# Kernel tuning notes

Measured on AMD Instinct MI355X. Metric: run time of the kernel, lower is better.

## Reference

```python
import jax, jax.numpy as jnp
import numpy as np
from jax import lax

N, C, RC, H, W = 2, 256, 32, 64, 64  # RC = C // 8


def conv1x1(x, w, b):
    # x: [n,c,h,w], w: [o,c], b: [o]
    return jnp.einsum('nchw,oc->nohw', x, w) + b[None, :, None, None]


def conv3x3(x, w, b):
    # x: [n,c,h,w], w: [o,i,3,3]
    y = lax.conv_general_dilated(x, w, window_strides=(1, 1), padding='SAME',
                                 dimension_numbers=('NCHW', 'OIHW', 'NCHW'))
    return y + b[None, :, None, None]


def setup_inputs() -> dict:
    key = jax.random.key(0)
    ks = jax.random.split(key, 16)
    p = lambda k, s: jax.random.normal(k, s, dtype=jnp.float32) * 0.02
    z = lambda o: jnp.zeros((o,), jnp.float32)
    return {
        'rgb_feat': jax.random.normal(ks[0], (N, C, H, W), jnp.float32),
        'chm_feat': jax.random.normal(ks[1], (N, C, H, W), jnp.float32),
        'rgb_q_w': p(ks[2], (RC, C)), 'rgb_q_b': z(RC),
        'rgb_k_w': p(ks[3], (RC, C)), 'rgb_k_b': z(RC),
        'rgb_v_w': p(ks[4], (C, C)), 'rgb_v_b': z(C),
        'depth_q_w': p(ks[5], (RC, C)), 'depth_q_b': z(RC),
        'depth_k_w': p(ks[6], (RC, C)), 'depth_k_b': z(RC),
        'depth_v_w': p(ks[7], (C, C)), 'depth_v_b': z(C),
        'gate_w': p(ks[8], (C, 2 * C)), 'gate_b': z(C),
        'fus1_w': p(ks[9], (2 * C, 2 * C)), 'fus1_b': z(2 * C),
        'fus2_w': p(ks[10], (2 * C, 2 * C, 3, 3)), 'fus2_b': z(2 * C),
        'fus3_w': p(ks[11], (C, 2 * C)), 'fus3_b': z(C),
        'skip_w': p(ks[12], (C, 2 * C)), 'skip_b': z(C),
    }


def reference(rgb_feat, chm_feat,
              rgb_q_w, rgb_q_b, rgb_k_w, rgb_k_b, rgb_v_w, rgb_v_b,
              depth_q_w, depth_q_b, depth_k_w, depth_k_b, depth_v_w, depth_v_b,
              gate_w, gate_b, fus1_w, fus1_b, fus2_w, fus2_b,
              fus3_w, fus3_b, skip_w, skip_b):
    n, c, h, w = rgb_feat.shape
    hw = h * w
    flat = lambda t: t.reshape(n, t.shape[1], hw)

    rq = flat(conv1x1(rgb_feat, rgb_q_w, rgb_q_b))       # [n,rc,hw]
    rk = flat(conv1x1(rgb_feat, rgb_k_w, rgb_k_b))       # [n,rc,hw]
    rv = flat(conv1x1(rgb_feat, rgb_v_w, rgb_v_b))       # [n,c,hw]
    dq = flat(conv1x1(chm_feat, depth_q_w, depth_q_b))   # [n,rc,hw]
    dk = flat(conv1x1(chm_feat, depth_k_w, depth_k_b))   # [n,rc,hw]
    dv = flat(conv1x1(chm_feat, depth_v_w, depth_v_b))   # [n,c,hw]

    # rgb branch attended with depth-derived attention
    rgb_attn = jax.nn.softmax(jnp.einsum('nri,nrj->nij', dq, dk), axis=-1)  # [n,hw,hw]
    br = jnp.einsum('nci,nij->ncj', rv, rgb_attn).reshape(rgb_feat.shape) + rgb_feat

    # depth branch attended with rgb-derived attention
    depth_attn = jax.nn.softmax(jnp.einsum('nri,nrj->nij', rq, rk), axis=-1)
    bd = jnp.einsum('nci,nij->ncj', dv, depth_attn).reshape(chm_feat.shape) + chm_feat

    cat = jnp.concatenate([br, bd], axis=1)              # [n,2c,h,w]
    g = jax.nn.sigmoid(conv1x1(cat, gate_w, gate_b))     # [n,c,h,w]
    c_fused = br * g + bd * (1.0 - g)
    d_fused = br * bd
    f = jnp.concatenate([c_fused, d_fused], axis=1)      # [n,2c,h,w]

    y = jax.nn.relu(conv1x1(f, fus1_w, fus1_b))
    y = jax.nn.relu(conv3x3(y, fus2_w, fus2_b))
    y = conv1x1(y, fus3_w, fus3_b)
    fused = y + conv1x1(f, skip_w, skip_b)
    return fused
```

## Files before the change

### kernel.cpp

```cpp
#include <hip/hip_runtime.h>
#include <stdint.h>


typedef __bf16 bf16_t;
typedef __bf16 bf16x8 __attribute__((ext_vector_type(8)));
typedef float f32x4 __attribute__((ext_vector_type(4)));

#define HW 4096
#define NB 2

__device__ inline f32x4 mfma_bf16(bf16x8 a, bf16x8 b, f32x4 c) {
    return __builtin_amdgcn_mfma_f32_16x16x32_bf16(a, b, c, 0, 0, 0);
}

#define MAXJOB 12
struct CvtJobs {
    const float* src[MAXJOB];
    bf16_t* dst[MAXJOB];
    int vend[MAXJOB];
    int rowlen[MAXJOB];
    int rowstride[MAXJOB];
    int rowoff[MAXJOB];
};

__global__ __launch_bounds__(256) void convert_batch_k(CvtJobs J, int totalvec) {
    int gv = blockIdx.x * 256 + threadIdx.x;
    if (gv >= totalvec) return;
    int j = 0;
    while (gv >= J.vend[j]) j++;
    int vbase = (j == 0) ? 0 : J.vend[j - 1];
    int e = (gv - vbase) * 8;
    const float* s = J.src[j] + e;
    float4 f0 = *(const float4*)s;
    float4 f1 = *(const float4*)(s + 4);
    bf16x8 o;
    o[0] = (bf16_t)f0.x; o[1] = (bf16_t)f0.y; o[2] = (bf16_t)f0.z; o[3] = (bf16_t)f0.w;
    o[4] = (bf16_t)f1.x; o[5] = (bf16_t)f1.y; o[6] = (bf16_t)f1.z; o[7] = (bf16_t)f1.w;
    int di = e;
    if (J.rowlen[j])
        di = (e / J.rowlen[j]) * J.rowstride[j] + J.rowoff[j] + (e % J.rowlen[j]);
    *(bf16x8*)(J.dst[j] + di) = o;
}

__global__ __launch_bounds__(256) void pack_bias_k(const float* qr, const float* kr,
                                                   const float* qd, const float* kd,
                                                   const float* sb, const float* fb,
                                                   float* BQK_R, float* BQK_D, float* BSUM) {
    int t = threadIdx.x;
    if (t < 32) {
        BQK_R[t] = qr[t]; BQK_R[32 + t] = kr[t];
        BQK_D[t] = qd[t]; BQK_D[32 + t] = kd[t];
    }
    BSUM[t] = sb[t] + fb[t];
}

__global__ __launch_bounds__(256) void reorder_fus2_k(const float* __restrict__ src,
                                                      bf16_t* __restrict__ dst) {
    int idx = blockIdx.x * 256 + threadIdx.x;
    if (idx >= 512 * 4608) return;
    int o = idx / 4608;
    int t = idx % 4608;
    int t9 = t / 512;
    int c  = t % 512;
    dst[idx] = (bf16_t)src[(size_t)o * 4608 + c * 9 + t9];
}

template <int EPI, bool OUT_BF16>
__global__ __launch_bounds__(256) void gemm_k(const bf16_t* __restrict__ A,
                                              const bf16_t* __restrict__ A2,
                                              const bf16_t* __restrict__ B,
                                              const float* __restrict__ bias,
                                              const float* __restrict__ bias2,
                                              void* __restrict__ outp,
                                              const void* __restrict__ aux,
                                              int M, int K, size_t strideB, size_t strideO) {
    __shared__ bf16_t Bt[64][72];
    const int t = threadIdx.x;
    const int mb = blockIdx.x, jb = blockIdx.y, n = blockIdx.z;
    const int w = t >> 6, lane = t & 63, quad = lane >> 4, l16 = lane & 15;

    const bf16_t* Au = (n >= 2) ? A2 : A;
    const float* biasu = (n >= 2) ? bias2 : bias;

    const bf16_t* Bb = B + (size_t)n * strideB + jb * 64;
    const int srow = t >> 2;
    const int scol = (t & 3) << 4;

    f32x4 zero = {0.f, 0.f, 0.f, 0.f};
    f32x4 acc[4] = {zero, zero, zero, zero};

    const bf16_t* Arow = Au + (size_t)(mb * 64 + w * 16 + l16) * K + quad * 8;

    for (int k0 = 0; k0 < K; k0 += 64) {
        const bf16_t* src = Bb + (size_t)(k0 + srow) * HW + scol;
        bf16x8 v0 = *(const bf16x8*)src;
        bf16x8 v1 = *(const bf16x8*)(src + 8);
        __syncthreads();
#pragma unroll
        for (int e = 0; e < 8; e++) Bt[scol + e][srow] = v0[e];
#pragma unroll
        for (int e = 0; e < 8; e++) Bt[scol + 8 + e][srow] = v1[e];
        __syncthreads();

        bf16x8 a0 = *(const bf16x8*)(Arow + k0);
        bf16x8 a1 = *(const bf16x8*)(Arow + k0 + 32);
#pragma unroll
        for (int ns = 0; ns < 4; ns++) {
            bf16x8 b0 = *(const bf16x8*)&Bt[ns * 16 + l16][quad * 8];
            bf16x8 b1 = *(const bf16x8*)&Bt[ns * 16 + l16][32 + quad * 8];
            acc[ns] = mfma_bf16(a0, b0, acc[ns]);
            acc[ns] = mfma_bf16(a1, b1, acc[ns]);
        }
    }

    if (EPI == 6) {
#pragma unroll
        for (int ns = 0; ns < 4; ns++) {
            int col = jb * 64 + ns * 16 + l16;
            union { bf16_t h[4]; unsigned long long u; } pk;
#pragma unroll
            for (int rr = 0; rr < 4; rr++) {
                int m = w * 16 + quad * 4 + rr;
                pk.h[rr] = (bf16_t)(acc[ns][rr] + biasu[m]);
            }
            *(unsigned long long*)((bf16_t*)outp +
                ((size_t)n * HW + col) * 64 + w * 16 + quad * 4) = pk.u;
        }
    } else if (EPI == 7) {
        const int m_base = mb * 64 + w * 16 + quad * 4;
#pragma unroll
        for (int ns = 0; ns < 4; ns++) {
            int col = jb * 64 + ns * 16 + l16;
            union { bf16_t h[4]; unsigned long long u; } pk;
#pragma unroll
            for (int rr = 0; rr < 4; rr++) {
                float v = acc[ns][rr] + biasu[m_base + rr];
                pk.h[rr] = (bf16_t)(v > 0.f ? v : 0.f);
            }
            *(unsigned long long*)((bf16_t*)outp +
                ((size_t)n * HW + col) * 512 + m_base) = pk.u;
        }
    } else if (EPI == 5) {
        const bf16_t* catp = (const bf16_t*)aux;
        bf16_t* f = (bf16_t*)outp;
#pragma unroll
        for (int ns = 0; ns < 4; ns++) {
#pragma unroll
            for (int rr = 0; rr < 4; rr++) {
                int m = mb * 64 + w * 16 + quad * 4 + rr;
                int col = jb * 64 + ns * 16 + l16;
                float v = acc[ns][rr] + biasu[m];
                float g = 1.f / (1.f + __expf(-v));
                size_t base = (size_t)n * 512 * HW + (size_t)m * HW + col;
                float br = (float)catp[base];
                float bd = (float)catp[base + (size_t)256 * HW];
                size_t ob = (size_t)n * 1024 * HW + (size_t)m * HW + col;
                f[ob] = (bf16_t)(br * g + bd * (1.f - g));
                f[ob + (size_t)256 * HW] = (bf16_t)(br * bd);
            }
        }
    } else {
#pragma unroll
        for (int ns = 0; ns < 4; ns++) {
#pragma unroll
            for (int rr = 0; rr < 4; rr++) {
                int m = mb * 64 + w * 16 + quad * 4 + rr;
                int col = jb * 64 + ns * 16 + l16;
                float v = acc[ns][rr] + biasu[m];
                if (EPI == 1) v = v > 0.f ? v : 0.f;
                size_t oi = (size_t)n * strideO + (size_t)m * HW + col;
                if (OUT_BF16) ((bf16_t*)outp)[oi] = (bf16_t)v;
                else ((float*)outp)[oi] = v;
            }
        }
    }
}

__global__ __launch_bounds__(256) void conv3_k(const bf16_t* __restrict__ A,
                                               const bf16_t* __restrict__ Y1n,
                                               const float* __restrict__ bias,
                                               bf16_t* __restrict__ outp,
                                               size_t strideN) {
    __shared__ bf16_t kTn[198][72];
    const int t = threadIdx.x;
    const int mb = blockIdx.x, y = blockIdx.y, n = blockIdx.z;
    const int w = t >> 6, lane = t & 63, quad = lane >> 4, l16 = lane & 15;

    f32x4 zero = {0.f, 0.f, 0.f, 0.f};
    f32x4 acc[2][4];
#pragma unroll
    for (int i = 0; i < 2; i++)
#pragma unroll
        for (int j = 0; j < 4; j++) acc[i][j] = zero;

    const bf16_t* Yb = Y1n + (size_t)n * HW * 512;

    const bf16_t* Arow0 = A + (size_t)(mb * 128 + w * 32 + l16) * 4608 + quad * 8;
    const bf16_t* Arow1 = Arow0 + (size_t)16 * 4608;

    int pxs[7], seg[7], gidx[7];
    bool ok[7], act[7];
#pragma unroll
    for (int i = 0; i < 7; i++) {
        int slot = t + i * 256;
        act[i] = slot < 1584;
        int ps = act[i] ? (slot >> 3) : 0;
        pxs[i] = ps;
        seg[i] = slot & 7;
        int r = ps / 66, xm = ps % 66;
        int yy = y + r - 1, xx = xm - 1;
        ok[i] = act[i] && ((unsigned)yy < 64u) && ((unsigned)xx < 64u);
        gidx[i] = ok[i] ? (yy * 64 + xx) : 0;
    }

    for (int c0 = 0; c0 < 512; c0 += 64) {
        bf16x8 vals[7];
#pragma unroll
        for (int i = 0; i < 7; i++) {
            bf16x8 v;
            if (ok[i]) {
                v = *(const bf16x8*)(Yb + (size_t)gidx[i] * 512 + c0 + seg[i] * 8);
            } else {
#pragma unroll
                for (int e = 0; e < 8; e++) v[e] = (bf16_t)0.f;
            }
            vals[i] = v;
        }
        __syncthreads();
#pragma unroll
        for (int i = 0; i < 7; i++)
            if (act[i]) *(bf16x8*)&kTn[pxs[i]][seg[i] * 8] = vals[i];
        __syncthreads();

#pragma unroll
        for (int t9 = 0; t9 < 9; t9++) {
            const int dy = t9 / 3, dx = t9 % 3;
            const bf16_t* ap0 = Arow0 + t9 * 512 + c0;
            const bf16_t* ap1 = Arow1 + t9 * 512 + c0;
            bf16x8 a00 = *(const bf16x8*)(ap0);
            bf16x8 a01 = *(const bf16x8*)(ap0 + 32);
            bf16x8 a10 = *(const bf16x8*)(ap1);
            bf16x8 a11 = *(const bf16x8*)(ap1 + 32);
#pragma unroll
            for (int ns = 0; ns < 4; ns++) {
                int p = dy * 66 + ns * 16 + l16 + dx;
                bf16x8 b0 = *(const bf16x8*)&kTn[p][quad * 8];
                bf16x8 b1 = *(const bf16x8*)&kTn[p][32 + quad * 8];
                acc[0][ns] = mfma_bf16(a00, b0, acc[0][ns]);
                acc[0][ns] = mfma_bf16(a01, b1, acc[0][ns]);
                acc[1][ns] = mfma_bf16(a10, b0, acc[1][ns]);
                acc[1][ns] = mfma_bf16(a11, b1, acc[1][ns]);
            }
        }
    }

#pragma unroll
    for (int ms = 0; ms < 2; ms++) {
#pragma unroll
        for (int ns = 0; ns < 4; ns++) {
#pragma unroll
            for (int rr = 0; rr < 4; rr++) {
                int m = mb * 128 + w * 32 + ms * 16 + quad * 4 + rr;
                int x = ns * 16 + l16;
                float v = acc[ms][ns][rr] + bias[m];
                v = v > 0.f ? v : 0.f;
                outp[(size_t)n * strideN + (size_t)m * HW + y * 64 + x] = (bf16_t)v;
            }
        }
    }
}

#define ATTN_STEP(P, AS, AV, ASN, AVN, ITN)                                    \
    {                                                                          \
        _Pragma("unroll")                                                      \
        for (int ns = 0; ns < 2; ns++) {                                       \
            f32x4 s = mfma_bf16(AS, bS[ns], zero);                             \
            union { bf16_t h[4]; unsigned long long u; } pk;                   \
            float zs = 0.f;                                                    \
            _Pragma("unroll")                                                  \
            for (int rr = 0; rr < 4; rr++) {                                   \
                pk.h[rr] = (bf16_t)__expf(s[rr]);                              \
                zs += (float)pk.h[rr];                                         \
            }                                                                  \
            zacc[ns] += zs;                                                    \
            *(unsigned long long*)&PT[P][ns * 16 + l16][w * 16 + quad * 4] = pk.u; \
        }                                                                      \
        ASN = *(const bf16x8*)(Qa + (size_t)(ITN) * (128 * 64));               \
        _Pragma("unroll")                                                      \
        for (int ks = 0; ks < 4; ks++) {                                       \
            AVN[0][ks] = *(const bf16x8*)(Vr0 + (size_t)(ITN) * 128 + ks * 32);\
            AVN[1][ks] = *(const bf16x8*)(Vr1 + (size_t)(ITN) * 128 + ks * 32);\
        }                                                                      \
        asm volatile("s_waitcnt lgkmcnt(0)" ::: "memory");                     \
        __builtin_amdgcn_s_barrier();                                          \
        __builtin_amdgcn_sched_barrier(0);                                     \
        __builtin_amdgcn_s_setprio(1);                                         \
        _Pragma("unroll")                                                      \
        for (int ns = 0; ns < 2; ns++) {                                       \
            _Pragma("unroll")                                                  \
            for (int ks = 0; ks < 4; ks++) {                                   \
                bf16x8 b = *(const bf16x8*)&PT[P][ns * 16 + l16][ks * 32 + quad * 8]; \
                acc[0][ns] = mfma_bf16(AV[0][ks], b, acc[0][ns]);              \
                acc[1][ns] = mfma_bf16(AV[1][ks], b, acc[1][ns]);              \
            }                                                                  \
        }                                                                      \
        __builtin_amdgcn_s_setprio(0);                                         \
    }

__global__ __launch_bounds__(512) void attn3_k(const bf16_t* __restrict__ QKT,
                                               const bf16_t* __restrict__ V,
                                               const float* __restrict__ rgb_feat,
                                               const float* __restrict__ chm_feat,
                                               bf16_t* __restrict__ CAT) {
    __shared__ bf16_t PT[2][32][136];
    __shared__ float Zp[8][32];
    const int t = threadIdx.x;
    const int lin = blockIdx.x + (blockIdx.y << 7);
    const int z = (lin >> 1) & 3;
    const int jb = ((lin >> 3) << 1) | (lin & 1);
    const int w = t >> 6, lane = t & 63, quad = lane >> 4, l16 = lane & 15;
    const int qs = z ^ 2, n = z & 1;

    const bf16_t* Q = QKT + (size_t)qs * HW * 64;

    bf16x8 bS[2];
#pragma unroll
    for (int ns = 0; ns < 2; ns++)
        bS[ns] = *(const bf16x8*)(Q + (size_t)(jb * 32 + ns * 16 + l16) * 64 + 32 + quad * 8);

    f32x4 zero = {0.f, 0.f, 0.f, 0.f};
    f32x4 acc[2][2];
#pragma unroll
    for (int i = 0; i < 2; i++)
#pragma unroll
        for (int j = 0; j < 2; j++) acc[i][j] = zero;
    float zacc[2] = {0.f, 0.f};

    const bf16_t* Vr0 = V + ((size_t)z * 256 + w * 16 + l16) * HW + quad * 8;
    const bf16_t* Vr1 = Vr0 + (size_t)128 * HW;
    const bf16_t* Qa = Q + (size_t)(w * 16 + l16) * 64 + quad * 8;

    bf16x8 aS0, aS1, aV0[2][4], aV1[2][4];
    aS0 = *(const bf16x8*)Qa;
#pragma unroll
    for (int ks = 0; ks < 4; ks++) {
        aV0[0][ks] = *(const bf16x8*)(Vr0 + ks * 32);
        aV0[1][ks] = *(const bf16x8*)(Vr1 + ks * 32);
    }

    for (int ii = 0; ii < 16; ii++) {
        const int it0 = 2 * ii;
        ATTN_STEP(0, aS0, aV0, aS1, aV1, it0 + 1);
        ATTN_STEP(1, aS1, aV1, aS0, aV0, (it0 + 2) & 31);
    }

#pragma unroll
    for (int ns = 0; ns < 2; ns++) {
        zacc[ns] += __shfl_xor(zacc[ns], 16, 64);
        zacc[ns] += __shfl_xor(zacc[ns], 32, 64);
    }
    if (lane < 16) { Zp[w][lane] = zacc[0]; Zp[w][16 + lane] = zacc[1]; }
    __syncthreads();
    float rz[2];
#pragma unroll
    for (int ns = 0; ns < 2; ns++) {
        float ssum = 0.f;
#pragma unroll
        for (int ww = 0; ww < 8; ww++) ssum += Zp[ww][ns * 16 + l16];
        rz[ns] = 1.f / ssum;
    }

    const float* feat = ((z < 2) ? rgb_feat : chm_feat) + (size_t)n * 256 * HW;
    bf16_t* outp = CAT + (size_t)n * 512 * HW + (size_t)(z < 2 ? 0 : 256) * HW;
#pragma unroll
    for (int ct = 0; ct < 2; ct++) {
#pragma unroll
        for (int ns = 0; ns < 2; ns++) {
#pragma unroll
            for (int rr = 0; rr < 4; rr++) {
                int c = ct * 128 + w * 16 + quad * 4 + rr;
                int col = jb * 32 + ns * 16 + l16;
                float v = acc[ct][ns][rr] * rz[ns] + feat[(size_t)c * HW + col];
                outp[(size_t)c * HW + col] = (bf16_t)v;
            }
        }
    }
}

extern "C" void kernel_launch(void* const* d_in, const int* in_sizes, int n_in,
                              void* d_out, int out_size, void* d_ws, size_t ws_size,
                              hipStream_t stream) {
    (void)in_sizes; (void)n_in; (void)out_size; (void)ws_size;

    const float* rgb_feat  = (const float*)d_in[0];
    const float* chm_feat  = (const float*)d_in[1];
    const float* rgb_q_w   = (const float*)d_in[2];
    const float* rgb_q_b   = (const float*)d_in[3];
    const float* rgb_k_w   = (const float*)d_in[4];
    const float* rgb_k_b   = (const float*)d_in[5];
    const float* rgb_v_w   = (const float*)d_in[6];
    const float* rgb_v_b   = (const float*)d_in[7];
    const float* depth_q_w = (const float*)d_in[8];
    const float* depth_q_b = (const float*)d_in[9];
    const float* depth_k_w = (const float*)d_in[10];
    const float* depth_k_b = (const float*)d_in[11];
    const float* depth_v_w = (const float*)d_in[12];
    const float* depth_v_b = (const float*)d_in[13];
    const float* gate_w    = (const float*)d_in[14];
    const float* gate_b    = (const float*)d_in[15];
    const float* fus1_w    = (const float*)d_in[16];
    const float* fus1_b    = (const float*)d_in[17];
    const float* fus2_w    = (const float*)d_in[18];
    const float* fus2_b    = (const float*)d_in[19];
    const float* fus3_w    = (const float*)d_in[20];
    const float* fus3_b    = (const float*)d_in[21];
    const float* skip_w    = (const float*)d_in[22];
    const float* skip_b    = (const float*)d_in[23];

    char* ws = (char*)d_ws;
    size_t off = 0;
    auto alloc = [&](size_t bytes) -> char* {
        char* p = ws + off;
        off += (bytes + 255) & ~(size_t)255;
        return p;
    };

    bf16_t* WQK_R = (bf16_t*)alloc(64 * 256 * 2);
    bf16_t* WQK_D = (bf16_t*)alloc(64 * 256 * 2);
    bf16_t* WV_R  = (bf16_t*)alloc(256 * 256 * 2);
    bf16_t* WV_D  = (bf16_t*)alloc(256 * 256 * 2);
    bf16_t* WGATE = (bf16_t*)alloc(256 * 512 * 2);
    bf16_t* WFUS1 = (bf16_t*)alloc(512 * 512 * 2);
    bf16_t* WFUS2 = (bf16_t*)alloc(512 * 4608 * 2);
    bf16_t* WCAT  = (bf16_t*)alloc(256 * 1024 * 2);
    float*  BQK_R = (float*)alloc(64 * 4);
    float*  BQK_D = (float*)alloc(64 * 4);
    float*  BSUM  = (float*)alloc(256 * 4);
    bf16_t* XB    = (bf16_t*)alloc((size_t)4 * 256 * HW * 2);
    bf16_t* QKT   = (bf16_t*)alloc((size_t)4 * HW * 64 * 2);
    bf16_t* V4    = (bf16_t*)alloc((size_t)4 * 256 * HW * 2);
    bf16_t* CAT   = (bf16_t*)alloc((size_t)NB * 512 * HW * 2);
    bf16_t* FY    = (bf16_t*)alloc((size_t)NB * 1024 * HW * 2);
    bf16_t* Y1    = (bf16_t*)alloc((size_t)NB * HW * 512 * 2);

    bf16_t* XR = XB;
    bf16_t* XC = XB + (size_t)2 * 256 * HW;

    CvtJobs J;
    int cum = 0, nj = 0;
    auto addjob = [&](const float* s, bf16_t* d, int cnt, int rl, int rs, int ro) {
        J.src[nj] = s; J.dst[nj] = d; cum += cnt / 8; J.vend[nj] = cum;
        J.rowlen[nj] = rl; J.rowstride[nj] = rs; J.rowoff[nj] = ro; nj++;
    };
    addjob(rgb_feat, XR, NB * 256 * HW, 0, 0, 0);
    addjob(chm_feat, XC, NB * 256 * HW, 0, 0, 0);
    addjob(rgb_q_w, WQK_R, 32 * 256, 0, 0, 0);
    addjob(rgb_k_w, WQK_R + 32 * 256, 32 * 256, 0, 0, 0);
    addjob(depth_q_w, WQK_D, 32 * 256, 0, 0, 0);
    addjob(depth_k_w, WQK_D + 32 * 256, 32 * 256, 0, 0, 0);
    addjob(rgb_v_w, WV_R, 256 * 256, 0, 0, 0);
    addjob(depth_v_w, WV_D, 256 * 256, 0, 0, 0);
    addjob(gate_w, WGATE, 256 * 512, 0, 0, 0);
    addjob(fus1_w, WFUS1, 512 * 512, 0, 0, 0);
    addjob(skip_w, WCAT, 256 * 512, 512, 1024, 0);
    addjob(fus3_w, WCAT, 256 * 512, 512, 1024, 512);
    int totalvec = cum;
    convert_batch_k<<<dim3((totalvec + 255) / 256), 256, 0, stream>>>(J, totalvec);
    reorder_fus2_k<<<dim3(512 * 4608 / 256), 256, 0, stream>>>(fus2_w, WFUS2);
    pack_bias_k<<<dim3(1), 256, 0, stream>>>(rgb_q_b, rgb_k_b, depth_q_b, depth_k_b,
                                             skip_b, fus3_b, BQK_R, BQK_D, BSUM);

    gemm_k<6, true><<<dim3(1, 64, 4), 256, 0, stream>>>(
        WQK_R, WQK_D, XB, BQK_R, BQK_D, QKT, nullptr, 64, 256, (size_t)256 * HW, 0);

    gemm_k<0, true><<<dim3(4, 64, 4), 256, 0, stream>>>(
        WV_R, WV_D, XB, rgb_v_b, depth_v_b, V4, nullptr, 256, 256, (size_t)256 * HW, (size_t)256 * HW);

    attn3_k<<<dim3(128, 4), 512, 0, stream>>>(QKT, V4, rgb_feat, chm_feat, CAT);

    gemm_k<5, true><<<dim3(4, 64, NB), 256, 0, stream>>>(
        WGATE, WGATE, CAT, gate_b, gate_b, FY, CAT, 256, 512, (size_t)512 * HW, 0);

    gemm_k<7, true><<<dim3(8, 64, NB), 256, 0, stream>>>(
        WFUS1, WFUS1, FY, fus1_b, fus1_b, Y1, nullptr, 512, 512, (size_t)1024 * HW, 0);

    conv3_k<<<dim3(4, 64, NB), 256, 0, stream>>>(WFUS2, Y1, fus2_b,
                                                 FY + (size_t)512 * HW, (size_t)1024 * HW);

    gemm_k<0, false><<<dim3(4, 64, NB), 256, 0, stream>>>(
        WCAT, WCAT, FY, BSUM, BSUM, d_out, nullptr, 256, 1024, (size_t)1024 * HW, (size_t)256 * HW);
}
```

Measured before the change: 401.5 us.

## Restructure attention kernel to split keys across waves, keeping P in registers

The attention kernel now gives each wave a contiguous quarter of the key range. It feeds the exponentiated scores straight from registers into 16x16x16 MFMAs, so the shared-memory round trip and the per-step barrier on P go away. Channels are split into two halves across twice as many 256-thread blocks. The per-wave partial outputs are reduced through a float shared-memory buffer at the end. In exchange, scores are recomputed once per channel half, register pressure rises (16 accumulators plus V prefetch), and a cross-wave reduction epilogue is added.

```diff
diff --git a/kernel.cpp b/kernel.cpp
--- a/kernel.cpp
+++ b/kernel.cpp
@@ -5,12 +5,16 @@
 typedef __bf16 bf16_t;
 typedef __bf16 bf16x8 __attribute__((ext_vector_type(8)));
 typedef float f32x4 __attribute__((ext_vector_type(4)));
+typedef short s16x4 __attribute__((ext_vector_type(4)));
 
 #define HW 4096
 #define NB 2
 
 __device__ inline f32x4 mfma_bf16(bf16x8 a, bf16x8 b, f32x4 c) {
     return __builtin_amdgcn_mfma_f32_16x16x32_bf16(a, b, c, 0, 0, 0);
+}
+__device__ inline f32x4 mfma16(s16x4 a, s16x4 b, f32x4 c) {
+    return __builtin_amdgcn_mfma_f32_16x16x16bf16_1k(a, b, c, 0, 0, 0);
 }
 
 #define MAXJOB 12
@@ -270,54 +274,51 @@
     }
 }
 
-#define ATTN_STEP(P, AS, AV, ASN, AVN, ITN)                                    \
-    {                                                                          \
-        _Pragma("unroll")                                                      \
-        for (int ns = 0; ns < 2; ns++) {                                       \
-            f32x4 s = mfma_bf16(AS, bS[ns], zero);                             \
-            union { bf16_t h[4]; unsigned long long u; } pk;                   \
-            float zs = 0.f;                                                    \
-            _Pragma("unroll")                                                  \
-            for (int rr = 0; rr < 4; rr++) {                                   \
-                pk.h[rr] = (bf16_t)__expf(s[rr]);                              \
-                zs += (float)pk.h[rr];                                         \
-            }                                                                  \
-            zacc[ns] += zs;                                                    \
-            *(unsigned long long*)&PT[P][ns * 16 + l16][w * 16 + quad * 4] = pk.u; \
-        }                                                                      \
-        ASN = *(const bf16x8*)(Qa + (size_t)(ITN) * (128 * 64));               \
-        _Pragma("unroll")                                                      \
-        for (int ks = 0; ks < 4; ks++) {                                       \
-            AVN[0][ks] = *(const bf16x8*)(Vr0 + (size_t)(ITN) * 128 + ks * 32);\
-            AVN[1][ks] = *(const bf16x8*)(Vr1 + (size_t)(ITN) * 128 + ks * 32);\
-        }                                                                      \
-        asm volatile("s_waitcnt lgkmcnt(0)" ::: "memory");                     \
-        __builtin_amdgcn_s_barrier();                                          \
-        __builtin_amdgcn_sched_barrier(0);                                     \
-        __builtin_amdgcn_s_setprio(1);                                         \
-        _Pragma("unroll")                                                      \
-        for (int ns = 0; ns < 2; ns++) {                                       \
-            _Pragma("unroll")                                                  \
-            for (int ks = 0; ks < 4; ks++) {                                   \
-                bf16x8 b = *(const bf16x8*)&PT[P][ns * 16 + l16][ks * 32 + quad * 8]; \
-                acc[0][ns] = mfma_bf16(AV[0][ks], b, acc[0][ns]);              \
-                acc[1][ns] = mfma_bf16(AV[1][ks], b, acc[1][ns]);              \
-            }                                                                  \
-        }                                                                      \
-        __builtin_amdgcn_s_setprio(0);                                         \
-    }
-
-__global__ __launch_bounds__(512) void attn3_k(const bf16_t* __restrict__ QKT,
+#define SSTEP(AS, SV)                                                          \
+    { SV[0] = mfma_bf16(AS, bS[0], zero); SV[1] = mfma_bf16(AS, bS[1], zero); }
+
+#define EXPPACK(SV, PB)                                                        \
+    { _Pragma("unroll")                                                        \
+      for (int ns = 0; ns < 2; ns++) {                                         \
+          union { bf16_t h[4]; s16x4 v; } pk;                                  \
+          float zs = 0.f;                                                      \
+          _Pragma("unroll")                                                    \
+          for (int rr = 0; rr < 4; rr++) {                                     \
+              pk.h[rr] = (bf16_t)__expf(SV[ns][rr]);                           \
+              zs += (float)pk.h[rr];                                           \
+          }                                                                    \
+          zacc[ns] += zs;                                                      \
+          PB[ns] = pk.v;                                                       \
+      } }
+
+#define PV16(AV, PB)                                                           \
+    { __builtin_amdgcn_s_setprio(1);                                           \
+      _Pragma("unroll")                                                        \
+      for (int ci = 0; ci < 8; ci++) {                                         \
+          acc[ci][0] = mfma16(AV[ci], PB[0], acc[ci][0]);                      \
+          acc[ci][1] = mfma16(AV[ci], PB[1], acc[ci][1]);                      \
+      }                                                                        \
+      __builtin_amdgcn_s_setprio(0); }
+
+#define LOADQ(DST, T) DST = *(const bf16x8*)(Qa + (size_t)((T) & 63) * (16 * 64));
+
+#define LOADV(DST, T)                                                          \
+    { _Pragma("unroll")                                                        \
+      for (int ci = 0; ci < 8; ci++)                                           \
+          DST[ci] = *(const s16x4*)(Vq + (size_t)ci * (16 * HW) + ((T) & 63) * 16); }
+
+__global__ __launch_bounds__(256) void attn3_k(const bf16_t* __restrict__ QKT,
                                                const bf16_t* __restrict__ V,
                                                const float* __restrict__ rgb_feat,
                                                const float* __restrict__ chm_feat,
                                                bf16_t* __restrict__ CAT) {
-    __shared__ bf16_t PT[2][32][136];
-    __shared__ float Zp[8][32];
+    __shared__ float OS[2][128][33];
+    __shared__ float Zp[4][32];
     const int t = threadIdx.x;
-    const int lin = blockIdx.x + (blockIdx.y << 7);
+    const int lin = blockIdx.x + (blockIdx.y << 8);
     const int z = (lin >> 1) & 3;
-    const int jb = ((lin >> 3) << 1) | (lin & 1);
+    const int u = ((lin >> 3) << 1) | (lin & 1);
+    const int cb = u & 1, jb = u >> 1;
     const int w = t >> 6, lane = t & 63, quad = lane >> 4, l16 = lane & 15;
     const int qs = z ^ 2, n = z & 1;
 
@@ -329,29 +330,39 @@
         bS[ns] = *(const bf16x8*)(Q + (size_t)(jb * 32 + ns * 16 + l16) * 64 + 32 + quad * 8);
 
     f32x4 zero = {0.f, 0.f, 0.f, 0.f};
-    f32x4 acc[2][2];
-#pragma unroll
-    for (int i = 0; i < 2; i++)
-#pragma unroll
-        for (int j = 0; j < 2; j++) acc[i][j] = zero;
+    f32x4 acc[8][2];
+#pragma unroll
+    for (int ci = 0; ci < 8; ci++) {
+        acc[ci][0] = zero; acc[ci][1] = zero;
+    }
     float zacc[2] = {0.f, 0.f};
 
-    const bf16_t* Vr0 = V + ((size_t)z * 256 + w * 16 + l16) * HW + quad * 8;
-    const bf16_t* Vr1 = Vr0 + (size_t)128 * HW;
-    const bf16_t* Qa = Q + (size_t)(w * 16 + l16) * 64 + quad * 8;
-
-    bf16x8 aS0, aS1, aV0[2][4], aV1[2][4];
-    aS0 = *(const bf16x8*)Qa;
-#pragma unroll
-    for (int ks = 0; ks < 4; ks++) {
-        aV0[0][ks] = *(const bf16x8*)(Vr0 + ks * 32);
-        aV0[1][ks] = *(const bf16x8*)(Vr1 + ks * 32);
-    }
-
-    for (int ii = 0; ii < 16; ii++) {
-        const int it0 = 2 * ii;
-        ATTN_STEP(0, aS0, aV0, aS1, aV1, it0 + 1);
-        ATTN_STEP(1, aS1, aV1, aS0, aV0, (it0 + 2) & 31);
+    const bf16_t* Qa = Q + (size_t)(w * 1024 + l16) * 64 + quad * 8;
+    const bf16_t* Vq = V + ((size_t)z * 256 + cb * 128 + l16) * HW + w * 1024 + quad * 4;
+
+    bf16x8 aSt, aS0, aS1;
+    s16x4 aVa[8], aVb[8], pba[2], pbb[2];
+    f32x4 sA[2], sB[2];
+    LOADQ(aSt, 0);
+    LOADV(aVa, 0);
+    LOADQ(aS0, 1);
+    LOADQ(aS1, 2);
+    LOADV(aVb, 1);
+    SSTEP(aSt, sA);
+    EXPPACK(sA, pba);
+
+    for (int tp = 0; tp < 32; tp++) {
+        const int tt = tp * 2;
+        SSTEP(aS0, sB);
+        PV16(aVa, pba);
+        LOADQ(aS0, tt + 3);
+        LOADV(aVa, tt + 2);
+        EXPPACK(sB, pbb);
+        SSTEP(aS1, sA);
+        PV16(aVb, pbb);
+        LOADQ(aS1, tt + 4);
+        LOADV(aVb, tt + 3);
+        EXPPACK(sA, pba);
     }
 
 #pragma unroll
@@ -360,30 +371,44 @@
         zacc[ns] += __shfl_xor(zacc[ns], 32, 64);
     }
     if (lane < 16) { Zp[w][lane] = zacc[0]; Zp[w][16 + lane] = zacc[1]; }
+
+    const int buf = w >> 1;
+    if ((w & 1) == 0) {
+#pragma unroll
+        for (int ci = 0; ci < 8; ci++)
+#pragma unroll
+            for (int ns = 0; ns < 2; ns++)
+#pragma unroll
+                for (int rr = 0; rr < 4; rr++)
+                    OS[buf][ci * 16 + quad * 4 + rr][ns * 16 + l16] = acc[ci][ns][rr];
+    }
     __syncthreads();
-    float rz[2];
-#pragma unroll
-    for (int ns = 0; ns < 2; ns++) {
-        float ssum = 0.f;
-#pragma unroll
-        for (int ww = 0; ww < 8; ww++) ssum += Zp[ww][ns * 16 + l16];
-        rz[ns] = 1.f / ssum;
-    }
-
+    if (w & 1) {
+#pragma unroll
+        for (int ci = 0; ci < 8; ci++)
+#pragma unroll
+            for (int ns = 0; ns < 2; ns++)
+#pragma unroll
+                for (int rr = 0; rr < 4; rr++)
+                    OS[buf][ci * 16 + quad * 4 + rr][ns * 16 + l16] += acc[ci][ns][rr];
+    }
+    __syncthreads();
+    for (int idx = t; idx < 128 * 33; idx += 256)
+        ((float*)OS[0])[idx] += ((float*)OS[1])[idx];
+    __syncthreads();
+
+    const int j = t & 31;
+    const int cl0 = (t >> 5) * 16;
+    const float Zj = Zp[0][j] + Zp[1][j] + Zp[2][j] + Zp[3][j];
+    const float rz = 1.f / Zj;
+    const int col = jb * 32 + j;
     const float* feat = ((z < 2) ? rgb_feat : chm_feat) + (size_t)n * 256 * HW;
     bf16_t* outp = CAT + (size_t)n * 512 * HW + (size_t)(z < 2 ? 0 : 256) * HW;
 #pragma unroll
-    for (int ct = 0; ct < 2; ct++) {
-#pragma unroll
-        for (int ns = 0; ns < 2; ns++) {
-#pragma unroll
-            for (int rr = 0; rr < 4; rr++) {
-                int c = ct * 128 + w * 16 + quad * 4 + rr;
-                int col = jb * 32 + ns * 16 + l16;
-                float v = acc[ct][ns][rr] * rz[ns] + feat[(size_t)c * HW + col];
-                outp[(size_t)c * HW + col] = (bf16_t)v;
-            }
-        }
+    for (int cc = 0; cc < 16; cc++) {
+        const int c = cb * 128 + cl0 + cc;
+        float v = OS[0][cl0 + cc][j] * rz + feat[(size_t)c * HW + col];
+        outp[(size_t)c * HW + col] = (bf16_t)v;
     }
 }
 
@@ -476,7 +501,7 @@
     gemm_k<0, true><<<dim3(4, 64, 4), 256, 0, stream>>>(
         WV_R, WV_D, XB, rgb_v_b, depth_v_b, V4, nullptr, 256, 256, (size_t)256 * HW, (size_t)256 * HW);
 
-    attn3_k<<<dim3(128, 4), 512, 0, stream>>>(QKT, V4, rgb_feat, chm_feat, CAT);
+    attn3_k<<<dim3(256, 4), 256, 0, stream>>>(QKT, V4, rgb_feat, chm_feat, CAT);
 
     gemm_k<5, true><<<dim3(4, 64, NB), 256, 0, stream>>>(
         WGATE, WGATE, CAT, gate_b, gate_b, FY, CAT, 256, 512, (size_t)512 * HW, 0);
```

Result: slower. 529.4 us (+31.8%).
